# Optimization experiments

Measured on AMD Instinct MI355X. Metric: run time of the kernel, lower is better.

The kernel has to match this reference:

```python
import jax, jax.numpy as jnp
import numpy as np

N_WIRES = 25                    # odd -> RX on wire 0, then SingleExcitation on (1,2),(3,4),...,(23,24)
DIM = 2 ** N_WIRES              # 33_554_432 amplitudes
N_THETA = (N_WIRES + 1) // 2    # 13


def _apply_rx(state, th, wire):
    """Apply RX(th) = [[cos, -i sin], [-i sin, cos]] (half-angle) to `wire`.
    PennyLane convention: wire 0 is the most-significant bit of the amplitude index."""
    c = jnp.cos(th * 0.5)
    ms = -1j * jnp.sin(th * 0.5)
    st = state.reshape(2 ** wire, 2, -1)          # [pre, 2, post]
    s0, s1 = st[:, 0], st[:, 1]
    new = jnp.stack([c * s0 + ms * s1, ms * s0 + c * s1], axis=1)
    return new.reshape(-1)


def _apply_single_excitation(state, phi, wire):
    """SingleExcitation(phi) on wires [wire, wire+1]: rotates the |01>,|10> subspace
    by angle phi/2; |00>,|11> untouched."""
    c = jnp.cos(phi * 0.5)
    s = jnp.sin(phi * 0.5)
    st = state.reshape(2 ** wire, 2, 2, -1)       # [pre, q_i, q_{i+1}, post]
    a00, a01, a10, a11 = st[:, 0, 0], st[:, 0, 1], st[:, 1, 0], st[:, 1, 1]
    n01 = c * a01 - s * a10
    n10 = s * a01 + c * a10
    new = jnp.stack([jnp.stack([a00, n01], axis=1),
                     jnp.stack([n10, a11], axis=1)], axis=1)
    return new.reshape(-1)


def setup_inputs() -> dict:
    key = jax.random.key(0)
    kf, kt = jax.random.split(key)
    feature = jax.random.normal(kf, (DIM,), dtype=jnp.float32)
    # he_normal init on shape (13, 1): std = sqrt(2 / fan_in) with fan_in = 13
    theta = jax.random.normal(kt, (N_THETA, 1), dtype=jnp.float32) * np.sqrt(2.0 / N_THETA)
    return {"feature": feature, "theta": theta}


def reference(feature, theta) -> jnp.ndarray:
    # AmplitudeEmbedding with pad_with=0.0: pad (no-op here, len == 2^n) then L2-normalize
    state = (feature / jnp.linalg.norm(feature)).astype(jnp.complex64)
    # odd wire count: RX(theta[0][0]) on wire 0, start pair gates at wire 1
    state = _apply_rx(state, theta[0, 0], 0)
    for i in range(1, N_WIRES, 2):                # i = 1,3,...,23 -> theta[0..11]
        state = _apply_single_excitation(state, theta[i // 2, 0], i)
    return jnp.real(state)
```

## Files before the change

kernel.cpp:

```cpp
#include <hip/hip_runtime.h>
#include <math.h>


typedef float f32x4 __attribute__((ext_vector_type(4)));

static __device__ __forceinline__ float4 nt_load4(const float* p) {
    f32x4 v = __builtin_nontemporal_load((const f32x4*)p);
    return *(float4*)&v;
}
static __device__ __forceinline__ void nt_store4(float* p, float4 v) {
    __builtin_nontemporal_store(*(f32x4*)&v, (f32x4*)p);
}

static __device__ __forceinline__ void bar_lgkm() {
    asm volatile("s_waitcnt lgkmcnt(0)\n\ts_barrier" ::: "memory");
}

static __device__ __forceinline__ void rot4(float4& a, float4& b, float c, float s) {
    float4 na, nb;
    na.x = c*a.x - s*b.x;  nb.x = s*a.x + c*b.x;
    na.y = c*a.y - s*b.y;  nb.y = s*a.y + c*b.y;
    na.z = c*a.z - s*b.z;  nb.z = s*a.z + c*b.z;
    na.w = c*a.w - s*b.w;  nb.w = s*a.w + c*b.w;
    a = na; b = nb;
}

static __device__ __forceinline__ float4 shflx4(float4 v, int m) {
    float4 r;
    r.x = __shfl_xor(v.x, m, 64);
    r.y = __shfl_xor(v.y, m, 64);
    r.z = __shfl_xor(v.z, m, 64);
    r.w = __shfl_xor(v.w, m, 64);
    return r;
}

template <int NR>
static __device__ __forceinline__ void rotshfl(float4* f, int sh, float c, float s, int lane) {
    const int pv = (lane >> sh) & 3;
    const bool act = (pv == 1) || (pv == 2);
    const float cl = act ? c : 1.0f;
    const float sl = act ? ((pv == 1) ? -s : s) : 0.0f;
    const int m = 3 << sh;
#pragma unroll
    for (int k = 0; k < NR; ++k) {
        float4 p = shflx4(f[k], m);
        float4 n;
        n.x = fmaf(sl, p.x, cl * f[k].x);
        n.y = fmaf(sl, p.y, cl * f[k].y);
        n.z = fmaf(sl, p.z, cl * f[k].z);
        n.w = fmaf(sl, p.w, cl * f[k].w);
        f[k] = n;
    }
}

static __device__ __forceinline__ float sumsq16(const float4* f) {
    float q[16];
#pragma unroll
    for (int k = 0; k < 16; ++k)
        q[k] = fmaf(f[k].x, f[k].x,
               fmaf(f[k].y, f[k].y,
               fmaf(f[k].z, f[k].z, f[k].w * f[k].w)));
#pragma unroll
    for (int st = 1; st < 16; st <<= 1)
#pragma unroll
        for (int i = 0; i < 16; i += (st << 1))
            q[i] += q[i + st];
    return q[0];
}

__global__ __launch_bounds__(256, 2) void qnn_p1(const float* __restrict__ in,
                                                 const float* __restrict__ theta,
                                                 float* __restrict__ out,
                                                 double* __restrict__ partials) {
    __shared__ __align__(16) float4 lds[4096];
    __shared__ double red[4];
    const int t = threadIdx.x, lane = t & 63, w2 = t >> 6;
    const int bid = blockIdx.x;
    const int h = bid >> 1, p = bid & 1;
    const long gA = ((long)h << 14) | (p ? (1L << 12) : 0);
    const long gB = ((long)h << 14) | (p ? (2L << 12) : (3L << 12));

    float c0,s0,c1,s1,c2,s2,c3,s3,c4,s4,c5,s5,c6,s6,c7,s7;
    { float th;
      th=0.5f*theta[11]; c0=cosf(th); s0=sinf(th);
      th=0.5f*theta[10]; c1=cosf(th); s1=sinf(th);
      th=0.5f*theta[9];  c2=cosf(th); s2=sinf(th);
      th=0.5f*theta[8];  c3=cosf(th); s3=sinf(th);
      th=0.5f*theta[7];  c4=cosf(th); s4=sinf(th);
      th=0.5f*theta[6];  c5=cosf(th); s5=sinf(th);
      th=0.5f*theta[5];  c6=cosf(th); s6=sinf(th);
      th=0.5f*theta[4];  c7=cosf(th); s7=sinf(th); }

    float4 f[16], g[16];
#pragma unroll
    for (int k = 0; k < 16; ++k)
        f[k] = nt_load4(in + ((gA + ((w2 << 10) | (k << 6) | lane)) << 2));
#pragma unroll
    for (int k = 0; k < 16; ++k)
        g[k] = nt_load4(in + ((gB + ((w2 << 10) | (k << 6) | lane)) << 2));

    const float sA = sumsq16(f);
    const float sB = sumsq16(g);

    if (p) {
#pragma unroll
        for (int k = 0; k < 16; ++k) rot4(f[k], g[k], c7, s7);
    }

#pragma unroll
    for (int k = 0; k < 16; ++k) {
        float ny = c0*f[k].y - s0*f[k].z;
        float nz = s0*f[k].y + c0*f[k].z;
        f[k].y = ny; f[k].z = nz;
    }
    rotshfl<16>(f, 0, c1, s1, lane);
    rotshfl<16>(f, 2, c2, s2, lane);
    rotshfl<16>(f, 4, c3, s3, lane);
#pragma unroll
    for (int hi = 0; hi < 16; hi += 4) rot4(f[hi+1], f[hi+2], c4, s4);
#pragma unroll
    for (int lo = 0; lo < 4; ++lo)     rot4(f[4+lo], f[8+lo], c5, s5);

#pragma unroll
    for (int k = 0; k < 16; ++k) lds[(w2 << 10) | (k << 6) | lane] = f[k];
    bar_lgkm();
#pragma unroll
    for (int m = 0; m < 16; ++m) f[m] = lds[(m << 8) | (w2 << 6) | lane];
#pragma unroll
    for (int lo = 0; lo < 4; ++lo) rot4(f[4+lo], f[8+lo], c6, s6);
#pragma unroll
    for (int m = 0; m < 16; ++m)
        *(float4*)(out + ((gA + ((m << 8) | (w2 << 6) | lane)) << 2)) = f[m];

#pragma unroll
    for (int k = 0; k < 16; ++k) {
        float ny = c0*g[k].y - s0*g[k].z;
        float nz = s0*g[k].y + c0*g[k].z;
        g[k].y = ny; g[k].z = nz;
    }
    rotshfl<16>(g, 0, c1, s1, lane);
    rotshfl<16>(g, 2, c2, s2, lane);
    rotshfl<16>(g, 4, c3, s3, lane);
#pragma unroll
    for (int hi = 0; hi < 16; hi += 4) rot4(g[hi+1], g[hi+2], c4, s4);
#pragma unroll
    for (int lo = 0; lo < 4; ++lo)     rot4(g[4+lo], g[8+lo], c5, s5);

    bar_lgkm();
#pragma unroll
    for (int k = 0; k < 16; ++k) lds[(w2 << 10) | (k << 6) | lane] = g[k];
    bar_lgkm();
#pragma unroll
    for (int m = 0; m < 16; ++m) g[m] = lds[(m << 8) | (w2 << 6) | lane];
#pragma unroll
    for (int lo = 0; lo < 4; ++lo) rot4(g[4+lo], g[8+lo], c6, s6);
#pragma unroll
    for (int m = 0; m < 16; ++m)
        *(float4*)(out + ((gB + ((m << 8) | (w2 << 6) | lane)) << 2)) = g[m];

    double acc = (double)sA + (double)sB;
#pragma unroll
    for (int off = 32; off > 0; off >>= 1) acc += __shfl_down(acc, off, 64);
    if (lane == 0) red[w2] = acc;
    bar_lgkm();
    if (t == 0)
        partials[bid] = red[0] + red[1] + red[2] + red[3];
}

__global__ void qnn_norm(const double* __restrict__ partials,
                         const float* __restrict__ theta,
                         double* __restrict__ scale) {
    __shared__ double w[4];
    const int t = threadIdx.x;
    double acc = 0.0;
    for (int i = t; i < 1024; i += 256) acc += partials[i];
#pragma unroll
    for (int off = 32; off > 0; off >>= 1) acc += __shfl_down(acc, off, 64);
    if ((t & 63) == 0) w[t >> 6] = acc;
    __syncthreads();
    if (t == 0) {
        double tot = w[0] + w[1] + w[2] + w[3];
        *scale = (double)cosf(0.5f * theta[0]) / sqrt(tot);
    }
}

__global__ __launch_bounds__(512, 2) void qnn_high(float* __restrict__ buf,
                                                   const float* __restrict__ theta,
                                                   const double* __restrict__ scale) {
    __shared__ __align__(16) float4 lds[8192];
    const int t = threadIdx.x;
    const int bid = blockIdx.x;
    const int f1514 = bid >> 7, mid = bid & 127;
    const long gqA = ((long)f1514 << 12) | ((long)mid << 5);
    const long gqB = gqA | (1L << 22);

    float c8,s8,c9,s9,c10,s10,c11,s11;
    { float th;
      th=0.5f*theta[3]; c8 =cosf(th); s8 =sinf(th);
      th=0.5f*theta[2]; c9 =cosf(th); s9 =sinf(th);
      th=0.5f*theta[1]; c10=cosf(th); s10=sinf(th);
      th=0.5f*theta[0]; c11=cosf(th); s11=sinf(th); }
    const float sc = (float)(*scale);

    const int rb = ((t >> 5) << 9) | (t & 31);

    float4 f[16], g[16];
#pragma unroll
    for (int k = 0; k < 16; ++k) {
        const int s_ = (k << 9) | t;
        f[k] = *(const float4*)(buf + ((gqA | ((long)(s_ >> 5) << 14) | (s_ & 31)) << 2));
    }
#pragma unroll
    for (int k = 0; k < 16; ++k) {
        const int s_ = (k << 9) | t;
        g[k] = *(const float4*)(buf + ((gqB | ((long)(s_ >> 5) << 14) | (s_ & 31)) << 2));
    }

#pragma unroll
    for (int q = 0; q < 16; q += 4) {
        rot4(f[q+1], f[q+2], c10, s10);
        rot4(g[q+1], g[q+2], c10, s10);
    }
#pragma unroll
    for (int lo = 0; lo < 4; ++lo) {
        rot4(f[4+lo], f[8+lo], c11, s11);
        rot4(g[4+lo], g[8+lo], c11, s11);
    }

#pragma unroll
    for (int k = 0; k < 16; ++k) lds[(k << 9) | t] = f[k];
    bar_lgkm();
#pragma unroll
    for (int m = 0; m < 16; ++m) f[m] = lds[rb | (m << 5)];
#pragma unroll
    for (int q = 0; q < 16; q += 4) rot4(f[q+1], f[q+2], c8, s8);
#pragma unroll
    for (int lo = 0; lo < 4; ++lo)  rot4(f[4+lo], f[8+lo], c9, s9);
#pragma unroll
    for (int m = 0; m < 16; ++m) {
        const int s_ = rb | (m << 5);
        float4 v = f[m];
        v.x *= sc; v.y *= sc; v.z *= sc; v.w *= sc;
        nt_store4(buf + ((gqA | ((long)(s_ >> 5) << 14) | (s_ & 31)) << 2), v);
    }
    bar_lgkm();

#pragma unroll
    for (int k = 0; k < 16; ++k) lds[(k << 9) | t] = g[k];
    bar_lgkm();
#pragma unroll
    for (int m = 0; m < 16; ++m) g[m] = lds[rb | (m << 5)];
#pragma unroll
    for (int q = 0; q < 16; q += 4) rot4(g[q+1], g[q+2], c8, s8);
#pragma unroll
    for (int lo = 0; lo < 4; ++lo)  rot4(g[4+lo], g[8+lo], c9, s9);
#pragma unroll
    for (int m = 0; m < 16; ++m) {
        const int s_ = rb | (m << 5);
        float4 v = g[m];
        v.x *= sc; v.y *= sc; v.z *= sc; v.w *= sc;
        nt_store4(buf + ((gqB | ((long)(s_ >> 5) << 14) | (s_ & 31)) << 2), v);
    }
}

extern "C" void kernel_launch(void* const* d_in, const int* in_sizes, int n_in,
                              void* d_out, int out_size, void* d_ws, size_t ws_size,
                              hipStream_t stream) {
    const float* in = (const float*)d_in[0];
    const float* theta = (const float*)d_in[1];
    float* out = (float*)d_out;
    double* part = (double*)d_ws;
    double* scale = part + 1024;

    qnn_p1<<<1024, 256, 0, stream>>>(in, theta, out, part);
    qnn_norm<<<1, 256, 0, stream>>>(part, theta, scale);
    qnn_high<<<512, 512, 0, stream>>>(out, theta, scale);
}
```

Baseline: 116.1 us.

## Move theta[4] pair gate from low-bit pass into high-bit pass

The gate on bits 12/13 (theta[4]) moves out of the first kernel and into the high-bit kernel, which now covers bits 12-21 plus the top-bit handling. The first kernel then uses contiguous 8192-amplitude tiles with no parity-dependent paired rotation. The high kernel's tile addressing is remapped so each block's strided loads span bits 12-20 instead of 14-22. Access patterns and the split of work between kernels change, and the gate-to-bit mapping must stay correct.

```diff
diff --git a/kernel.cpp b/kernel.cpp
--- a/kernel.cpp
+++ b/kernel.cpp
@@ -75,12 +75,10 @@
     __shared__ __align__(16) float4 lds[4096];
     __shared__ double red[4];
     const int t = threadIdx.x, lane = t & 63, w2 = t >> 6;
-    const int bid = blockIdx.x;
-    const int h = bid >> 1, p = bid & 1;
-    const long gA = ((long)h << 14) | (p ? (1L << 12) : 0);
-    const long gB = ((long)h << 14) | (p ? (2L << 12) : (3L << 12));
-
-    float c0,s0,c1,s1,c2,s2,c3,s3,c4,s4,c5,s5,c6,s6,c7,s7;
+    const long gA = (long)blockIdx.x << 13;
+    const long gB = gA + 4096;
+
+    float c0,s0,c1,s1,c2,s2,c3,s3,c4,s4,c5,s5,c6,s6;
     { float th;
       th=0.5f*theta[11]; c0=cosf(th); s0=sinf(th);
       th=0.5f*theta[10]; c1=cosf(th); s1=sinf(th);
@@ -88,8 +86,7 @@
       th=0.5f*theta[8];  c3=cosf(th); s3=sinf(th);
       th=0.5f*theta[7];  c4=cosf(th); s4=sinf(th);
       th=0.5f*theta[6];  c5=cosf(th); s5=sinf(th);
-      th=0.5f*theta[5];  c6=cosf(th); s6=sinf(th);
-      th=0.5f*theta[4];  c7=cosf(th); s7=sinf(th); }
+      th=0.5f*theta[5];  c6=cosf(th); s6=sinf(th); }
 
     float4 f[16], g[16];
 #pragma unroll
@@ -100,12 +97,6 @@
         g[k] = nt_load4(in + ((gB + ((w2 << 10) | (k << 6) | lane)) << 2));
 
     const float sA = sumsq16(f);
-    const float sB = sumsq16(g);
-
-    if (p) {
-#pragma unroll
-        for (int k = 0; k < 16; ++k) rot4(f[k], g[k], c7, s7);
-    }
 
 #pragma unroll
     for (int k = 0; k < 16; ++k) {
@@ -132,6 +123,7 @@
     for (int m = 0; m < 16; ++m)
         *(float4*)(out + ((gA + ((m << 8) | (w2 << 6) | lane)) << 2)) = f[m];
 
+    const float sB = sumsq16(g);
 #pragma unroll
     for (int k = 0; k < 16; ++k) {
         float ny = c0*g[k].y - s0*g[k].z;
@@ -164,7 +156,7 @@
     if (lane == 0) red[w2] = acc;
     bar_lgkm();
     if (t == 0)
-        partials[bid] = red[0] + red[1] + red[2] + red[3];
+        partials[blockIdx.x] = red[0] + red[1] + red[2] + red[3];
 }
 
 __global__ void qnn_norm(const double* __restrict__ partials,
@@ -190,12 +182,13 @@
     __shared__ __align__(16) float4 lds[8192];
     const int t = threadIdx.x;
     const int bid = blockIdx.x;
-    const int f1514 = bid >> 7, mid = bid & 127;
-    const long gqA = ((long)f1514 << 12) | ((long)mid << 5);
-    const long gqB = gqA | (1L << 22);
-
-    float c8,s8,c9,s9,c10,s10,c11,s11;
+    const int b24 = bid >> 8, p = (bid >> 7) & 1, mid = bid & 127;
+    const long baseA = ((long)b24 << 22) | (p ? (1L << 20) : 0)        | ((long)mid << 5);
+    const long baseB = ((long)b24 << 22) | (p ? (2L << 20) : (3L << 20)) | ((long)mid << 5);
+
+    float c7,s7,c8,s8,c9,s9,c10,s10,c11,s11;
     { float th;
+      th=0.5f*theta[4]; c7 =cosf(th); s7 =sinf(th);
       th=0.5f*theta[3]; c8 =cosf(th); s8 =sinf(th);
       th=0.5f*theta[2]; c9 =cosf(th); s9 =sinf(th);
       th=0.5f*theta[1]; c10=cosf(th); s10=sinf(th);
@@ -208,23 +201,27 @@
 #pragma unroll
     for (int k = 0; k < 16; ++k) {
         const int s_ = (k << 9) | t;
-        f[k] = *(const float4*)(buf + ((gqA | ((long)(s_ >> 5) << 14) | (s_ & 31)) << 2));
+        f[k] = *(const float4*)(buf + ((baseA | ((long)(s_ >> 5) << 12) | (s_ & 31)) << 2));
     }
 #pragma unroll
     for (int k = 0; k < 16; ++k) {
         const int s_ = (k << 9) | t;
-        g[k] = *(const float4*)(buf + ((gqB | ((long)(s_ >> 5) << 14) | (s_ & 31)) << 2));
-    }
-
+        g[k] = *(const float4*)(buf + ((baseB | ((long)(s_ >> 5) << 12) | (s_ & 31)) << 2));
+    }
+
+    if (p) {
+#pragma unroll
+        for (int k = 0; k < 16; ++k) rot4(f[k], g[k], c11, s11);
+    }
 #pragma unroll
     for (int q = 0; q < 16; q += 4) {
-        rot4(f[q+1], f[q+2], c10, s10);
-        rot4(g[q+1], g[q+2], c10, s10);
+        rot4(f[q+1], f[q+2], c9, s9);
+        rot4(g[q+1], g[q+2], c9, s9);
     }
 #pragma unroll
     for (int lo = 0; lo < 4; ++lo) {
-        rot4(f[4+lo], f[8+lo], c11, s11);
-        rot4(g[4+lo], g[8+lo], c11, s11);
+        rot4(f[4+lo], f[8+lo], c10, s10);
+        rot4(g[4+lo], g[8+lo], c10, s10);
     }
 
 #pragma unroll
@@ -233,15 +230,15 @@
 #pragma unroll
     for (int m = 0; m < 16; ++m) f[m] = lds[rb | (m << 5)];
 #pragma unroll
-    for (int q = 0; q < 16; q += 4) rot4(f[q+1], f[q+2], c8, s8);
-#pragma unroll
-    for (int lo = 0; lo < 4; ++lo)  rot4(f[4+lo], f[8+lo], c9, s9);
+    for (int q = 0; q < 16; q += 4) rot4(f[q+1], f[q+2], c7, s7);
+#pragma unroll
+    for (int lo = 0; lo < 4; ++lo)  rot4(f[4+lo], f[8+lo], c8, s8);
 #pragma unroll
     for (int m = 0; m < 16; ++m) {
         const int s_ = rb | (m << 5);
         float4 v = f[m];
         v.x *= sc; v.y *= sc; v.z *= sc; v.w *= sc;
-        nt_store4(buf + ((gqA | ((long)(s_ >> 5) << 14) | (s_ & 31)) << 2), v);
+        nt_store4(buf + ((baseA | ((long)(s_ >> 5) << 12) | (s_ & 31)) << 2), v);
     }
     bar_lgkm();
 
@@ -251,15 +248,15 @@
 #pragma unroll
     for (int m = 0; m < 16; ++m) g[m] = lds[rb | (m << 5)];
 #pragma unroll
-    for (int q = 0; q < 16; q += 4) rot4(g[q+1], g[q+2], c8, s8);
-#pragma unroll
-    for (int lo = 0; lo < 4; ++lo)  rot4(g[4+lo], g[8+lo], c9, s9);
+    for (int q = 0; q < 16; q += 4) rot4(g[q+1], g[q+2], c7, s7);
+#pragma unroll
+    for (int lo = 0; lo < 4; ++lo)  rot4(g[4+lo], g[8+lo], c8, s8);
 #pragma unroll
     for (int m = 0; m < 16; ++m) {
         const int s_ = rb | (m << 5);
         float4 v = g[m];
         v.x *= sc; v.y *= sc; v.z *= sc; v.w *= sc;
-        nt_store4(buf + ((gqB | ((long)(s_ >> 5) << 14) | (s_ & 31)) << 2), v);
+        nt_store4(buf + ((baseB | ((long)(s_ >> 5) << 12) | (s_ & 31)) << 2), v);
     }
 }
 
```

Result: faster. 95.26 us (-18.0%).
